# Kernel tuning notes

Measured on AMD Instinct MI355X. Metric: run time of the kernel, lower is better.

Reference implementation:

```python
import jax, jax.numpy as jnp
import numpy as np
import math

_PHI = (1.0 + 5.0 ** 0.5) / 2.0
_VERTS_RAW = np.array([(-1, _PHI, 0), (1, _PHI, 0), (-1, -_PHI, 0), (1, -_PHI, 0),
                       (0, -1, _PHI), (0, 1, _PHI), (0, -1, -_PHI), (0, 1, -_PHI),
                       (_PHI, 0, -1), (_PHI, 0, 1), (-_PHI, 0, -1), (-_PHI, 0, 1)], dtype=np.float32)
_VERTS = _VERTS_RAW / np.linalg.norm(_VERTS_RAW, axis=1, keepdims=True)
_FACES = [(0,11,5),(0,5,1),(0,1,7),(0,7,10),(0,10,11),(1,5,9),(5,11,4),(11,10,2),(10,7,6),(7,1,8),
          (3,9,4),(3,4,2),(3,2,6),(3,6,8),(3,8,9),(4,9,5),(2,4,11),(6,2,10),(8,6,7),(9,8,1)]

def _build_edges():
    es = set()
    for f in _FACES:
        for i in range(3):
            es.add(tuple(sorted((f[i], f[(i + 1) % 3]))))
    return np.array(sorted(es), dtype=np.int32)

_EDGES = _build_edges()  # [30, 2] undirected edges of the icosahedron


def _grid_mapping(lat, lon):
    # Mirrors IcosahedralFlowMatch._grid_mapping exactly (incl. the view/permute quirk).
    lat_c = jnp.linspace(-math.pi / 2, math.pi / 2, lat)
    lon_c = jnp.linspace(-math.pi, math.pi, lon)
    lon_g, lat_g = jnp.meshgrid(lon_c, lat_c, indexing='xy')  # each [lat, lon]
    flat = jnp.stack([lat_g, lon_g], axis=-1).reshape(-1, 2)  # [G, 2]
    verts = jnp.asarray(_VERTS)
    vlat = jnp.arcsin(verts[:, 2])
    vlon = jnp.arctan2(verts[:, 1], verts[:, 0])
    dlat = flat[None, :, 0] - vlat[:, None]
    dlon = jnp.remainder(flat[None, :, 1] - vlon[:, None] + math.pi, 2 * math.pi) - math.pi
    d2 = dlat ** 2 + dlon ** 2                            # [12, G]
    vert_to_grid = jnp.argmin(d2, axis=1)                 # [12] nearest grid cell per vertex
    grid_to_vert = jnp.argmin(d2, axis=0)                 # [G] nearest vertex per grid cell
    grid_to_vert = grid_to_vert.reshape(lon, lat).T       # torch: .view(lon,lat).permute(1,0)
    return vert_to_grid, grid_to_vert


def setup_inputs() -> dict:
    key = jax.random.key(0)
    ks = jax.random.split(key, 8)
    B, C, H, W = 16, 4, 721, 1440
    D, L = 256, 4
    s = 0.02
    return {
        'x': jax.random.normal(ks[0], (B, C, H, W), jnp.float32),
        't': jax.random.uniform(ks[1], (B,), dtype=jnp.float32),
        'W_in': jax.random.normal(ks[2], (C, D), jnp.float32) * s,
        'b_in': jnp.zeros((D,), jnp.float32),
        'W_layers': jax.random.normal(ks[3], (L, D, D), jnp.float32) * s,
        'b_layers': jax.random.normal(ks[4], (L, D), jnp.float32) * s,
        'W_out': jax.random.normal(ks[5], (D, C), jnp.float32) * s,
        'b_out': jnp.zeros((C,), jnp.float32),
    }


def reference(x, t, W_in, b_in, W_layers, b_layers, W_out, b_out):
    B, C, H, W = x.shape
    v2g, g2v = _grid_mapping(H, W)
    nodes = x.transpose(0, 2, 3, 1).reshape(B, H * W, C)   # [B, G, C]
    feats = nodes[:, v2g, :]                               # [B, 12, C] gather vertex features
    hn = feats @ W_in + b_in                               # [B, 12, D]
    src = jnp.asarray(_EDGES[:, 0])
    dst = jnp.asarray(_EDGES[:, 1])
    n_verts = _VERTS.shape[0]
    deg = jnp.zeros((n_verts,), hn.dtype).at[dst].add(1.0).at[src].add(1.0)
    deg = jnp.maximum(deg, 1.0)[None, :, None]
    for i in range(W_layers.shape[0]):                     # fixed n_layers=4
        agg = jnp.zeros_like(hn).at[:, dst, :].add(hn[:, src, :]).at[:, src, :].add(hn[:, dst, :])
        agg = agg / deg
        hn = hn + jax.nn.relu(agg @ W_layers[i] + b_layers[i])
    out_nodes = hn @ W_out + b_out                         # [B, 12, C]
    out = out_nodes[:, g2v.reshape(-1), :].reshape(B, H, W, C).transpose(0, 3, 1, 2)
    return out
```

## Files before the change

### kernel.cpp

```cpp
#include <hip/hip_runtime.h>
#include <math.h>

#define HH 721
#define WW 1440
#define HWV (HH*WW)
#define NB 16
#define NC 4
#define ND 256
#define NL 4
#define NQ (HWV/4)

#define PHI_F 1.61803398874989484820458683436564f

typedef float vfloat4 __attribute__((ext_vector_type(4)));

__constant__ float c_rx[12] = {-1.f, 1.f, -1.f, 1.f,  0.f, 0.f, 0.f, 0.f,
                               PHI_F, PHI_F, -PHI_F, -PHI_F};
__constant__ float c_ry[12] = {PHI_F, PHI_F, -PHI_F, -PHI_F, -1.f, 1.f, -1.f, 1.f,
                               0.f, 0.f, 0.f, 0.f};
__constant__ float c_rz[12] = {0.f, 0.f, 0.f, 0.f, PHI_F, PHI_F, -PHI_F, -PHI_F,
                               -1.f, 1.f, -1.f, 1.f};
__constant__ int c_nbr[12][5] = {
    {11, 5, 1, 7, 10}, {0, 5, 7, 9, 8}, {11, 10, 3, 4, 6}, {9, 4, 2, 6, 8},
    {5, 11, 3, 9, 2},  {0, 11, 1, 9, 4}, {10, 7, 3, 2, 8}, {0, 1, 10, 6, 8},
    {7, 1, 3, 6, 9},   {1, 5, 3, 4, 8},  {0, 7, 11, 2, 6}, {0, 5, 10, 4, 2}};

__device__ __forceinline__ void vert_latlon(int v, double* olat, double* olon) {
#pragma clang fp contract(off)
  const float P = PHI_F;
  float n = sqrtf(1.0f + P * P);
  float xf = c_rx[v] / n;
  float yf = c_ry[v] / n;
  float zf = c_rz[v] / n;
  *olat = asin((double)zf);
  *olon = atan2((double)yf, (double)xf);
}

__device__ __forceinline__ double grid_lat(int i) {
#pragma clang fp contract(off)
  if (i == 720) return M_PI / 2;
  double v = (double)i * (M_PI / 720.0);
  return v - M_PI / 2;
}

__device__ __forceinline__ double grid_lon(int j) {
#pragma clang fp contract(off)
  if (j == 1439) return M_PI;
  double v = (double)j * (2.0 * M_PI / 1439.0);
  return v - M_PI;
}

__device__ __forceinline__ double d2f(double lat, double lon, double vlat,
                                      double vlon) {
#pragma clang fp contract(off)
  double dlat = lat - vlat;
  double x = (lon - vlon) + M_PI;
  const double TP = 2.0 * M_PI;
  double r = (x < 0.0) ? (x + TP) : ((x >= TP) ? (x - TP) : x);
  double dlon = r - M_PI;
  return dlat * dlat + dlon * dlon;
}

__global__ __launch_bounds__(1024) void gnn_kernel(
    const float* __restrict__ x, const float* __restrict__ W_in,
    const float* __restrict__ b_in, const float* __restrict__ W_layers,
    const float* __restrict__ b_layers, const float* __restrict__ W_out,
    const float* __restrict__ b_out, float* __restrict__ out_tbl) {
  __shared__ int s_v2g[12];
  __shared__ float s_feats[12][4];
  __shared__ float s_hn[12][ND];
  __shared__ float s_agg[12][ND];
  const int b = blockIdx.x;
  const int t = threadIdx.x;
  const int g = t >> 8;
  const int d = t & (ND - 1);
  const int n0 = g * 3;

  if (t < 12) {
    double vlat, vlon;
    vert_latlon(t, &vlat, &vlon);
    int i0 = (int)floor((vlat + M_PI / 2) / (M_PI / 720.0) + 0.5);
    int j0 = (int)floor((vlon + M_PI) / (2.0 * M_PI / 1439.0) + 0.5);
    int cand[11] = {0, 1, 2, 1437, 1438, 1439, j0 - 2, j0 - 1, j0, j0 + 1, j0 + 2};
    for (int a = 6; a < 11; a++) {
      if (cand[a] < 0) cand[a] = 0;
      if (cand[a] > 1439) cand[a] = 1439;
    }
    for (int a = 1; a < 11; a++) {
      int key = cand[a];
      int p = a - 1;
      while (p >= 0 && cand[p] > key) {
        cand[p + 1] = cand[p];
        p--;
      }
      cand[p + 1] = key;
    }
    double best = 1e300;
    int bi = 0;
    for (int ii = i0 - 2; ii <= i0 + 2; ii++) {
      if (ii < 0 || ii > 720) continue;
      double lat = grid_lat(ii);
      int prev = -1;
      for (int a = 0; a < 11; a++) {
        int j = cand[a];
        if (j == prev) continue;
        prev = j;
        double dq = d2f(lat, grid_lon(j), vlat, vlon);
        if (dq < best) {
          best = dq;
          bi = ii * 1440 + j;
        }
      }
    }
    s_v2g[t] = bi;
  }
  __syncthreads();

  if (t < 48) {
    int n = t >> 2, c = t & 3;
    int k = s_v2g[n];
    s_feats[n][c] = x[(size_t)(b * NC + c) * HWV + k];
  }
  __syncthreads();

#pragma unroll
  for (int nn = 0; nn < 3; nn++) {
    int n = n0 + nn;
    float s = b_in[d];
#pragma unroll
    for (int c = 0; c < 4; c++) s += s_feats[n][c] * W_in[c * ND + d];
    s_hn[n][d] = s;
  }
  __syncthreads();

  for (int l = 0; l < NL; l++) {
#pragma unroll
    for (int nn = 0; nn < 3; nn++) {
      int n = n0 + nn;
      float s = 0.f;
#pragma unroll
      for (int e = 0; e < 5; e++) s += s_hn[c_nbr[n][e]][d];
      s_agg[n][d] = s / 5.0f;
    }
    __syncthreads();

    float acc0 = 0.f, acc1 = 0.f, acc2 = 0.f;
    const float* Wl = W_layers + (size_t)l * ND * ND + d;
#pragma unroll 8
    for (int dd = 0; dd < ND; dd += 4) {
      vfloat4 a0 = *(const vfloat4*)&s_agg[n0 + 0][dd];
      vfloat4 a1 = *(const vfloat4*)&s_agg[n0 + 1][dd];
      vfloat4 a2 = *(const vfloat4*)&s_agg[n0 + 2][dd];
      float w0 = Wl[(size_t)(dd + 0) * ND];
      float w1 = Wl[(size_t)(dd + 1) * ND];
      float w2 = Wl[(size_t)(dd + 2) * ND];
      float w3 = Wl[(size_t)(dd + 3) * ND];
      acc0 += a0.x * w0; acc0 += a0.y * w1; acc0 += a0.z * w2; acc0 += a0.w * w3;
      acc1 += a1.x * w0; acc1 += a1.y * w1; acc1 += a1.z * w2; acc1 += a1.w * w3;
      acc2 += a2.x * w0; acc2 += a2.y * w1; acc2 += a2.z * w2; acc2 += a2.w * w3;
    }
    float bb = b_layers[l * ND + d];
    {
      float u0 = acc0 + bb;
      float u1 = acc1 + bb;
      float u2 = acc2 + bb;
      s_hn[n0 + 0][d] += (u0 > 0.f) ? u0 : 0.f;
      s_hn[n0 + 1][d] += (u1 > 0.f) ? u1 : 0.f;
      s_hn[n0 + 2][d] += (u2 > 0.f) ? u2 : 0.f;
    }
    __syncthreads();
  }

  if (t < 48) {
    int n = t >> 2, c = t & 3;
    float s = b_out[c];
    for (int dd = 0; dd < ND; dd++) s += s_hn[n][dd] * W_out[dd * 4 + c];
    out_tbl[b * 48 + c * 12 + n] = s;
  }
}

__global__ __launch_bounds__(256) void scatter_kernel(
    const float* __restrict__ tbl_g, float* __restrict__ out) {
  __shared__ float s_tbl[NB * NC * 12];
  __shared__ double svlat[12], svlon[12];
  const int t = threadIdx.x;
  if (t < 12) {
    double a, o;
    vert_latlon(t, &a, &o);
    svlat[t] = a;
    svlon[t] = o;
  }
  for (int i = t; i < NB * NC * 12; i += 256) s_tbl[i] = tbl_g[i];
  __syncthreads();

  int q = blockIdx.x * 256 + t;
  if (q >= NQ) return;
  int h = q / 360;
  int w4 = (q - h * 360) * 4;

  int v[4];
#pragma unroll
  for (int s2 = 0; s2 < 4; s2++) {
    int kk = (w4 + s2) * 721 + h;
    int i2 = kk / 1440;
    int j2 = kk - i2 * 1440;
    double lat = grid_lat(i2);
    double lon = grid_lon(j2);
    double best = 1e300;
    int bv = 0;
#pragma unroll
    for (int vv = 0; vv < 12; vv++) {
      double dd = d2f(lat, lon, svlat[vv], svlon[vv]);
      if (dd < best) {
        best = dd;
        bv = vv;
      }
    }
    if (i2 == 360 && bv >= 8) bv ^= 1;
    v[s2] = bv;
  }

  vfloat4* out4 = (vfloat4*)out;
#pragma unroll
  for (int b = 0; b < NB; b++) {
#pragma unroll
    for (int c = 0; c < NC; c++) {
      const float* tb = &s_tbl[b * 48 + c * 12];
      vfloat4 val = {tb[v[0]], tb[v[1]], tb[v[2]], tb[v[3]]};
      __builtin_nontemporal_store(val, &out4[(size_t)(b * 4 + c) * NQ + q]);
    }
  }
}

extern "C" void kernel_launch(void* const* d_in, const int* in_sizes, int n_in,
                              void* d_out, int out_size, void* d_ws,
                              size_t ws_size, hipStream_t stream) {
  const float* x = (const float*)d_in[0];
  const float* W_in = (const float*)d_in[2];
  const float* b_in = (const float*)d_in[3];
  const float* W_layers = (const float*)d_in[4];
  const float* b_layers = (const float*)d_in[5];
  const float* W_out = (const float*)d_in[6];
  const float* b_out = (const float*)d_in[7];
  float* out = (float*)d_out;
  float* tbl = (float*)d_ws;

  gnn_kernel<<<NB, 1024, 0, stream>>>(x, W_in, b_in, W_layers, b_layers, W_out,
                                      b_out, tbl);
  int blocks = (NQ + 255) / 256;
  scatter_kernel<<<blocks, 256, 0, stream>>>(tbl, out);
}
```

Baseline: 481.9 us.

## Split GNN into per-layer kernels parallel over batch and vertex

Replaces the single 16-block GNN kernel with a separate grid-mapping kernel, an input-projection kernel and one launch per layer. The layer launches run 192 blocks, one per batch/vertex pair, with hidden states ping-ponging through global workspace. Vertex lat/lon values are computed once and stored in the workspace, so the scatter kernel reads them instead of recomputing asin/atan2 in every block. This spreads the serial GNN stage across more compute units but adds several launches and extra global round-trips, and each block now re-reads the full layer weights.

```diff
diff --git a/kernel.cpp b/kernel.cpp
--- a/kernel.cpp
+++ b/kernel.cpp
@@ -11,6 +11,12 @@
 #define NQ (HWV/4)
 
 #define PHI_F 1.61803398874989484820458683436564f
+
+#define WS_V2G 0
+#define WS_VLL 64
+#define WS_TBL 512
+#define WS_HNA 4096
+#define WS_HNB (4096 + NB*12*ND*4)
 
 typedef float vfloat4 __attribute__((ext_vector_type(4)));
 
@@ -61,134 +67,124 @@
   return dlat * dlat + dlon * dlon;
 }
 
-__global__ __launch_bounds__(1024) void gnn_kernel(
+__global__ __launch_bounds__(64) void map_kernel(char* __restrict__ ws) {
+  const int t = threadIdx.x;
+  if (t >= 12) return;
+  int* v2g = (int*)(ws + WS_V2G);
+  double* vll = (double*)(ws + WS_VLL);
+  double vlat, vlon;
+  vert_latlon(t, &vlat, &vlon);
+  vll[t] = vlat;
+  vll[12 + t] = vlon;
+  int i0 = (int)floor((vlat + M_PI / 2) / (M_PI / 720.0) + 0.5);
+  int j0 = (int)floor((vlon + M_PI) / (2.0 * M_PI / 1439.0) + 0.5);
+  int cand[11] = {0, 1, 2, 1437, 1438, 1439, j0 - 2, j0 - 1, j0, j0 + 1, j0 + 2};
+  for (int a = 6; a < 11; a++) {
+    if (cand[a] < 0) cand[a] = 0;
+    if (cand[a] > 1439) cand[a] = 1439;
+  }
+  for (int a = 1; a < 11; a++) {
+    int key = cand[a];
+    int p = a - 1;
+    while (p >= 0 && cand[p] > key) {
+      cand[p + 1] = cand[p];
+      p--;
+    }
+    cand[p + 1] = key;
+  }
+  double best = 1e300;
+  int bi = 0;
+  for (int ii = i0 - 2; ii <= i0 + 2; ii++) {
+    if (ii < 0 || ii > 720) continue;
+    double lat = grid_lat(ii);
+    int prev = -1;
+    for (int a = 0; a < 11; a++) {
+      int j = cand[a];
+      if (j == prev) continue;
+      prev = j;
+      double dq = d2f(lat, grid_lon(j), vlat, vlon);
+      if (dq < best) {
+        best = dq;
+        bi = ii * 1440 + j;
+      }
+    }
+  }
+  v2g[t] = bi;
+}
+
+__global__ __launch_bounds__(256) void init_kernel(
     const float* __restrict__ x, const float* __restrict__ W_in,
-    const float* __restrict__ b_in, const float* __restrict__ W_layers,
-    const float* __restrict__ b_layers, const float* __restrict__ W_out,
-    const float* __restrict__ b_out, float* __restrict__ out_tbl) {
-  __shared__ int s_v2g[12];
-  __shared__ float s_feats[12][4];
-  __shared__ float s_hn[12][ND];
-  __shared__ float s_agg[12][ND];
-  const int b = blockIdx.x;
-  const int t = threadIdx.x;
-  const int g = t >> 8;
-  const int d = t & (ND - 1);
-  const int n0 = g * 3;
-
-  if (t < 12) {
-    double vlat, vlon;
-    vert_latlon(t, &vlat, &vlon);
-    int i0 = (int)floor((vlat + M_PI / 2) / (M_PI / 720.0) + 0.5);
-    int j0 = (int)floor((vlon + M_PI) / (2.0 * M_PI / 1439.0) + 0.5);
-    int cand[11] = {0, 1, 2, 1437, 1438, 1439, j0 - 2, j0 - 1, j0, j0 + 1, j0 + 2};
-    for (int a = 6; a < 11; a++) {
-      if (cand[a] < 0) cand[a] = 0;
-      if (cand[a] > 1439) cand[a] = 1439;
-    }
-    for (int a = 1; a < 11; a++) {
-      int key = cand[a];
-      int p = a - 1;
-      while (p >= 0 && cand[p] > key) {
-        cand[p + 1] = cand[p];
-        p--;
-      }
-      cand[p + 1] = key;
-    }
-    double best = 1e300;
-    int bi = 0;
-    for (int ii = i0 - 2; ii <= i0 + 2; ii++) {
-      if (ii < 0 || ii > 720) continue;
-      double lat = grid_lat(ii);
-      int prev = -1;
-      for (int a = 0; a < 11; a++) {
-        int j = cand[a];
-        if (j == prev) continue;
-        prev = j;
-        double dq = d2f(lat, grid_lon(j), vlat, vlon);
-        if (dq < best) {
-          best = dq;
-          bi = ii * 1440 + j;
-        }
-      }
-    }
-    s_v2g[t] = bi;
-  }
+    const float* __restrict__ b_in, char* __restrict__ ws) {
+  __shared__ float s_f[4];
+  const int blk = blockIdx.x;
+  const int b = blk / 12, n = blk % 12;
+  const int t = threadIdx.x;
+  const int* v2g = (const int*)(ws + WS_V2G);
+  float* hnA = (float*)(ws + WS_HNA);
+  if (t < 4) s_f[t] = x[(size_t)(b * NC + t) * HWV + v2g[n]];
   __syncthreads();
-
-  if (t < 48) {
-    int n = t >> 2, c = t & 3;
-    int k = s_v2g[n];
-    s_feats[n][c] = x[(size_t)(b * NC + c) * HWV + k];
-  }
+  float s = b_in[t];
+#pragma unroll
+  for (int c = 0; c < 4; c++) s += s_f[c] * W_in[c * ND + t];
+  hnA[(size_t)(b * 12 + n) * ND + t] = s;
+}
+
+__global__ __launch_bounds__(256) void layer_kernel(
+    const float* __restrict__ hsrc, float* __restrict__ hdst,
+    const float* __restrict__ Wl, const float* __restrict__ bl,
+    const float* __restrict__ W_out, const float* __restrict__ b_out,
+    float* __restrict__ tbl, int do_out) {
+  __shared__ float s_agg[ND];
+  __shared__ float s_hn[ND];
+  const int blk = blockIdx.x;
+  const int b = blk / 12, n = blk % 12;
+  const int t = threadIdx.x;
+
+  float a = 0.f;
+#pragma unroll
+  for (int e = 0; e < 5; e++)
+    a += hsrc[(size_t)(b * 12 + c_nbr[n][e]) * ND + t];
+  s_agg[t] = a / 5.0f;
+  float hold = hsrc[(size_t)(b * 12 + n) * ND + t];
   __syncthreads();
 
-#pragma unroll
-  for (int nn = 0; nn < 3; nn++) {
-    int n = n0 + nn;
-    float s = b_in[d];
-#pragma unroll
-    for (int c = 0; c < 4; c++) s += s_feats[n][c] * W_in[c * ND + d];
-    s_hn[n][d] = s;
-  }
-  __syncthreads();
-
-  for (int l = 0; l < NL; l++) {
-#pragma unroll
-    for (int nn = 0; nn < 3; nn++) {
-      int n = n0 + nn;
-      float s = 0.f;
-#pragma unroll
-      for (int e = 0; e < 5; e++) s += s_hn[c_nbr[n][e]][d];
-      s_agg[n][d] = s / 5.0f;
-    }
+  float acc = 0.f;
+  const float* W = Wl + t;
+#pragma unroll 8
+  for (int dd = 0; dd < ND; dd += 4) {
+    vfloat4 a4 = *(const vfloat4*)&s_agg[dd];
+    float w0 = W[(size_t)(dd + 0) * ND];
+    float w1 = W[(size_t)(dd + 1) * ND];
+    float w2 = W[(size_t)(dd + 2) * ND];
+    float w3 = W[(size_t)(dd + 3) * ND];
+    acc += a4.x * w0; acc += a4.y * w1; acc += a4.z * w2; acc += a4.w * w3;
+  }
+  float u = acc + bl[t];
+  float hnew = hold + ((u > 0.f) ? u : 0.f);
+  hdst[(size_t)(b * 12 + n) * ND + t] = hnew;
+
+  if (do_out) {
+    s_hn[t] = hnew;
     __syncthreads();
-
-    float acc0 = 0.f, acc1 = 0.f, acc2 = 0.f;
-    const float* Wl = W_layers + (size_t)l * ND * ND + d;
-#pragma unroll 8
-    for (int dd = 0; dd < ND; dd += 4) {
-      vfloat4 a0 = *(const vfloat4*)&s_agg[n0 + 0][dd];
-      vfloat4 a1 = *(const vfloat4*)&s_agg[n0 + 1][dd];
-      vfloat4 a2 = *(const vfloat4*)&s_agg[n0 + 2][dd];
-      float w0 = Wl[(size_t)(dd + 0) * ND];
-      float w1 = Wl[(size_t)(dd + 1) * ND];
-      float w2 = Wl[(size_t)(dd + 2) * ND];
-      float w3 = Wl[(size_t)(dd + 3) * ND];
-      acc0 += a0.x * w0; acc0 += a0.y * w1; acc0 += a0.z * w2; acc0 += a0.w * w3;
-      acc1 += a1.x * w0; acc1 += a1.y * w1; acc1 += a1.z * w2; acc1 += a1.w * w3;
-      acc2 += a2.x * w0; acc2 += a2.y * w1; acc2 += a2.z * w2; acc2 += a2.w * w3;
-    }
-    float bb = b_layers[l * ND + d];
-    {
-      float u0 = acc0 + bb;
-      float u1 = acc1 + bb;
-      float u2 = acc2 + bb;
-      s_hn[n0 + 0][d] += (u0 > 0.f) ? u0 : 0.f;
-      s_hn[n0 + 1][d] += (u1 > 0.f) ? u1 : 0.f;
-      s_hn[n0 + 2][d] += (u2 > 0.f) ? u2 : 0.f;
-    }
-    __syncthreads();
-  }
-
-  if (t < 48) {
-    int n = t >> 2, c = t & 3;
-    float s = b_out[c];
-    for (int dd = 0; dd < ND; dd++) s += s_hn[n][dd] * W_out[dd * 4 + c];
-    out_tbl[b * 48 + c * 12 + n] = s;
+    if (t < 4) {
+      int c = t;
+      float s = b_out[c];
+      for (int dd = 0; dd < ND; dd++) s += s_hn[dd] * W_out[dd * 4 + c];
+      tbl[b * 48 + c * 12 + n] = s;
+    }
   }
 }
 
 __global__ __launch_bounds__(256) void scatter_kernel(
-    const float* __restrict__ tbl_g, float* __restrict__ out) {
+    const char* __restrict__ ws, float* __restrict__ out) {
   __shared__ float s_tbl[NB * NC * 12];
   __shared__ double svlat[12], svlon[12];
   const int t = threadIdx.x;
+  const double* vll = (const double*)(ws + WS_VLL);
+  const float* tbl_g = (const float*)(ws + WS_TBL);
   if (t < 12) {
-    double a, o;
-    vert_latlon(t, &a, &o);
-    svlat[t] = a;
-    svlon[t] = o;
+    svlat[t] = vll[t];
+    svlon[t] = vll[12 + t];
   }
   for (int i = t; i < NB * NC * 12; i += 256) s_tbl[i] = tbl_g[i];
   __syncthreads();
@@ -243,10 +239,23 @@
   const float* W_out = (const float*)d_in[6];
   const float* b_out = (const float*)d_in[7];
   float* out = (float*)d_out;
-  float* tbl = (float*)d_ws;
-
-  gnn_kernel<<<NB, 1024, 0, stream>>>(x, W_in, b_in, W_layers, b_layers, W_out,
-                                      b_out, tbl);
+  char* ws = (char*)d_ws;
+  float* tbl = (float*)(ws + WS_TBL);
+  float* hnA = (float*)(ws + WS_HNA);
+  float* hnB = (float*)(ws + WS_HNB);
+
+  map_kernel<<<1, 64, 0, stream>>>(ws);
+  init_kernel<<<NB * 12, 256, 0, stream>>>(x, W_in, b_in, ws);
+  const float* hs = hnA;
+  float* hd = hnB;
+  for (int l = 0; l < NL; l++) {
+    layer_kernel<<<NB * 12, 256, 0, stream>>>(
+        hs, hd, W_layers + (size_t)l * ND * ND, b_layers + (size_t)l * ND,
+        W_out, b_out, tbl, (l == NL - 1) ? 1 : 0);
+    const float* tmp = hd;
+    hd = (float*)hs;
+    hs = tmp;
+  }
   int blocks = (NQ + 255) / 256;
-  scatter_kernel<<<blocks, 256, 0, stream>>>(tbl, out);
-}
+  scatter_kernel<<<blocks, 256, 0, stream>>>(ws, out);
+}
```

After: 442.9 us. -8.1%, faster.
